# Performance work log

Hardware: AMD Instinct MI355X
Metric: run time of the kernel (lower is better)

The kernel has to match this reference:

```python
import jax, jax.numpy as jnp
import numpy as np

N_NODES = 50000
N_FEAT = 63          # nodeChannels C = N_FEAT + 1 = 64
N_EDGES = 800000
N_LABELS = 10000
BATCH = 4
N_LAYERS = 5
C = N_FEAT + 1


def setup_inputs() -> dict:
    key = jax.random.key(0)
    ks = jax.random.split(key, 16)
    s = 0.05  # small init scale for numerical sanity
    return {
        "cov": jax.random.normal(ks[0], (BATCH, N_LABELS), jnp.float32),
        "nodes": jax.random.normal(ks[1], (N_NODES, N_FEAT), jnp.float32),
        "edges": jax.random.randint(ks[2], (2, N_EDGES), 0, N_NODES, jnp.int64 if jax.config.jax_enable_x64 else jnp.int32),
        "count2label": jnp.arange(N_LABELS, dtype=jnp.int32),
        "ggc_weight": jax.random.normal(ks[3], (N_LAYERS, C, C), jnp.float32) * s,
        "gru_w_ih": jax.random.normal(ks[4], (3 * C, C), jnp.float32) * s,
        "gru_w_hh": jax.random.normal(ks[5], (3 * C, C), jnp.float32) * s,
        "gru_b_ih": jax.random.normal(ks[6], (3 * C,), jnp.float32) * s,
        "gru_b_hh": jax.random.normal(ks[7], (3 * C,), jnp.float32) * s,
        "ai_w": jax.random.normal(ks[8], (2 * C, 2 * C), jnp.float32) * s,
        "ai_b": jax.random.normal(ks[9], (2 * C,), jnp.float32) * s,
        "aj_w": jax.random.normal(ks[10], (2 * C, 2 * C), jnp.float32) * s,
        "aj_b": jax.random.normal(ks[11], (2 * C,), jnp.float32) * s,
        "mlp_w": jax.random.normal(ks[12], (256, 2 * C), jnp.float32) * s,
        "mlp_b": jax.random.normal(ks[13], (256,), jnp.float32) * s,
        "critic_w": jax.random.normal(ks[14], (1, 256), jnp.float32) * s,
        "critic_b": jax.random.normal(ks[15], (1,), jnp.float32) * s,
    }


def _gru_cell(m, h, w_ih, w_hh, b_ih, b_hh):
    # torch GRUCell, gate order r, z, n
    gx = m @ w_ih.T + b_ih   # [..., 3C]
    gh = h @ w_hh.T + b_hh
    c = h.shape[-1]
    xr, xz, xn = gx[..., :c], gx[..., c:2 * c], gx[..., 2 * c:]
    hr, hz, hn = gh[..., :c], gh[..., c:2 * c], gh[..., 2 * c:]
    r = jax.nn.sigmoid(xr + hr)
    z = jax.nn.sigmoid(xz + hz)
    n = jnp.tanh(xn + r * hn)
    return (1.0 - z) * n + z * h


def reference(cov, nodes, edges, count2label, ggc_weight,
              gru_w_ih, gru_w_hh, gru_b_ih, gru_b_hh,
              ai_w, ai_b, aj_w, aj_b, mlp_w, mlp_b, critic_w, critic_b):
    n, f = nodes.shape
    b = cov.shape[0]
    # scatter coverage into per-graph node channel: covInGraph[count2label] = cov
    cov_in_graph = jnp.zeros((b, n), cov.dtype).at[:, count2label].set(cov)
    # batched node input [B, N, C]; batched graph = B identical copies w/ offset edges
    x0 = jnp.concatenate(
        [jnp.broadcast_to(nodes, (b, n, f)), cov_in_graph[..., None]], axis=-1)
    src, dst = edges[0], edges[1]

    def scatter_add(mb):  # [N, C] -> [N, C]: sum messages from source at target
        return jax.ops.segment_sum(mb[src], dst, num_segments=n)

    x = x0
    for i in range(ggc_weight.shape[0]):
        m = x @ ggc_weight[i]                     # dense per-layer matmul [B,N,C]
        agg = jax.vmap(scatter_add)(m)            # edge scatter-add propagate
        x = _gru_cell(agg, x, gru_w_ih, gru_w_hh, gru_b_ih, gru_b_hh)

    # attention gate: sigmoid(Wi cat) * relu(Wj cat), cat = [x, x0]
    cat = jnp.concatenate([x, x0], axis=-1)       # [B, N, 2C]
    att = jax.nn.sigmoid(cat @ ai_w.T + ai_b) * jax.nn.relu(cat @ aj_w.T + aj_b)
    pooled = jax.nn.relu(att.sum(axis=1))         # global_add_pool -> [B, 2C]
    state = jax.nn.relu(pooled @ mlp_w.T + mlp_b) # graphmlp
    return state @ critic_w.T + critic_b          # critic value [B, 1]
```

## Files before the change

kernel.cpp:

```cpp
#include <hip/hip_runtime.h>
#include <math.h>

#define NN 50000
#define NF 63
#define NE 800000
#define NL 10000
#define NB 4
#define NLAY 5
#define BN (NB*NN)
#define NTILES (BN/64)
#define SCAN_NBLK ((NN+255)/256)
#define HIST_NBLK ((NE+255)/256)

using f32x4  = __attribute__((ext_vector_type(4))) float;
using f32x2  = __attribute__((ext_vector_type(2))) float;
using bf16x8 = __attribute__((ext_vector_type(8))) __bf16;

__device__ __forceinline__ float frcp(float x){ return __builtin_amdgcn_rcpf(x); }
__device__ __forceinline__ float sigm(float v){ return frcp(1.f + __expf(-v)); }
__device__ __forceinline__ float tanh_f(float v){ return fmaf(-2.f, frcp(__expf(2.f*v) + 1.f), 1.f); }

__device__ __forceinline__ ushort f2bf(float f){
    uint u = __builtin_bit_cast(uint, f);
    u += 0x7fffu + ((u >> 16) & 1u);
    return (ushort)(u >> 16);
}
__device__ __forceinline__ float bf_lo(uint v){ return __builtin_bit_cast(float, v << 16); }
__device__ __forceinline__ float bfu(ushort v){ return __builtin_bit_cast(float, ((uint)v) << 16); }

__device__ __forceinline__ uchar f2fp8(float v){
    int enc = __builtin_amdgcn_cvt_pk_fp8_f32(v, v, 0, false);
    return (uchar)(enc & 0xff);
}

__device__ __forceinline__ bf16x8 ldfrag(const ushort* p){
    uint4 v = *(const uint4*)p;
    return __builtin_bit_cast(bf16x8, v);
}
__device__ __forceinline__ f32x4 MFMA(bf16x8 a, bf16x8 b, f32x4 c){
    return __builtin_amdgcn_mfma_f32_16x16x32_bf16(a, b, c, 0, 0, 0);
}

__global__ void k_setup(const int* __restrict__ edges, int* __restrict__ cnt,
                        const float* __restrict__ wih, const float* __restrict__ whh,
                        const float* __restrict__ aiw, const float* __restrict__ ajw,
                        const float* __restrict__ ggc,
                        ushort* __restrict__ whhb, ushort* __restrict__ aiwb,
                        ushort* __restrict__ ajwb, ushort* __restrict__ wfb){
    int bid = blockIdx.x;
    if (bid < HIST_NBLK){
        int e = bid*256 + threadIdx.x;
        if (e < NE) atomicAdd(&cnt[edges[NE + e]], 1);
        return;
    }
    int i = (bid - HIST_NBLK)*256 + threadIdx.x;
    if (i < 12288)        whhb[i]        = f2bf(whh[i]);
    else if (i < 28672)   aiwb[i-12288]  = f2bf(aiw[i-12288]);
    else if (i < 45056)   ajwb[i-28672]  = f2bf(ajw[i-28672]);
    else if (i < 106496){
        int t = i - 45056;
        int lay = t / 12288;
        int rem = t % 12288;
        int n = rem >> 6, k = rem & 63;
        const float* W  = ggc + lay*4096 + k*64;
        const float* wr = wih + n*64;
        float s = 0.f;
        #pragma unroll 8
        for (int c = 0; c < 64; ++c) s = fmaf(W[c], wr[c], s);
        wfb[t] = f2bf(s);
    }
}

__global__ void k_scan1(const int* __restrict__ cnt, int* __restrict__ tmp, int* __restrict__ bsum){
    __shared__ int sh[256];
    int tx = threadIdx.x, i = blockIdx.x*256 + tx;
    int v = (i < NN) ? cnt[i] : 0;
    sh[tx] = v; __syncthreads();
    for (int off = 1; off < 256; off <<= 1){
        int u = (tx >= off) ? sh[tx-off] : 0;
        __syncthreads();
        sh[tx] += u;
        __syncthreads();
    }
    int incl = sh[tx];
    if (i < NN) tmp[i] = incl - v;
    if (tx == 255) bsum[blockIdx.x] = incl;
}

__global__ void k_scan2(const int* __restrict__ bsum, int* __restrict__ boff){
    __shared__ int sh[256];
    int tx = threadIdx.x;
    int v = (tx < SCAN_NBLK) ? bsum[tx] : 0;
    sh[tx] = v; __syncthreads();
    for (int off = 1; off < 256; off <<= 1){
        int u = (tx >= off) ? sh[tx-off] : 0;
        __syncthreads();
        sh[tx] += u;
        __syncthreads();
    }
    boff[tx] = sh[tx] - v;
}

__global__ void k_scan3(const int* __restrict__ tmp, const int* __restrict__ boff,
                        int* __restrict__ row_start, int* __restrict__ cursor){
    int i = blockIdx.x*256 + threadIdx.x;
    if (i < NN){
        int rs = tmp[i] + boff[blockIdx.x];
        row_start[i] = rs;
        cursor[i] = rs;
    }
    if (i == 0) row_start[NN] = NE;
}

__global__ void k_fillcsr(const int* __restrict__ edges, int* __restrict__ cursor, int* __restrict__ csr_src){
    int e = blockIdx.x*256 + threadIdx.x;
    if (e < NE){
        int d = edges[NE + e];
        int pos = atomicAdd(&cursor[d], 1);
        csr_src[pos] = edges[e];
    }
}

__global__ void k_x0(const float* __restrict__ nodes, ushort* __restrict__ x0I,
                     uchar* __restrict__ x0F){
    int f = blockIdx.x*256 + threadIdx.x;
    int row = f >> 4, c4 = f & 15;
    int n = row % NN, b = row / NN;
    float v[4];
    #pragma unroll
    for (int i = 0; i < 4; ++i){
        int c = c4*4 + i;
        v[i] = (c < NF) ? nodes[(size_t)n*NF + c] : 0.f;
    }
    uint2 pk;
    pk.x = (uint)f2bf(v[0]) | ((uint)f2bf(v[1]) << 16);
    pk.y = (uint)f2bf(v[2]) | ((uint)f2bf(v[3]) << 16);
    *(uint2*)(x0I + ((size_t)n*4 + b)*64 + c4*4) = pk;
    if (b == 0){
        uint q = 0;
        q = (uint)__builtin_amdgcn_cvt_pk_fp8_f32(v[0], v[1], (int)q, false);
        q = (uint)__builtin_amdgcn_cvt_pk_fp8_f32(v[2], v[3], (int)q, true);
        *(uint*)(x0F + (size_t)n*64 + c4*4) = q;
    }
}

__global__ void k_cov(const float* __restrict__ cov, const int* __restrict__ c2l,
                      ushort* __restrict__ x0I, ushort* __restrict__ covB){
    int i = blockIdx.x*256 + threadIdx.x;
    if (i < NB*NL){
        int b = i / NL, j = i % NL;
        int nd = c2l[j];
        ushort vb = f2bf(cov[i]);
        x0I[((size_t)nd*4 + b)*64 + 63] = vb;
        covB[(size_t)nd*4 + b] = vb;
    }
}

__global__ __launch_bounds__(256) void k_agg0(const uchar* __restrict__ x0F,
                                              const ushort* __restrict__ covB,
                                              const int* __restrict__ row_start,
                                              const int* __restrict__ csr_src,
                                              ushort* __restrict__ aggx){
    int tx = threadIdx.x, l = tx & 63, w = tx >> 6;
    int d = __builtin_amdgcn_readfirstlane(blockIdx.x*4 + w);
    int h = l >> 4;
    int t = l & 15;
    const uint off = (uint)(t*4);
    int e0 = row_start[d], e1 = row_start[d+1];
    float a0=0.f,a1=0.f,a2=0.f,a3=0.f,c=0.f;
    int e = e0 + h;
    for (; e + 12 < e1; e += 16){
        int s[4];
        #pragma unroll
        for (int j = 0; j < 4; ++j) s[j] = csr_src[e + 4*j];
        uint v[4];
        #pragma unroll
        for (int j = 0; j < 4; ++j) v[j] = *(const uint*)(x0F + (size_t)s[j]*64 + off);
        #pragma unroll
        for (int j = 0; j < 4; ++j){
            f32x2 p;
            p = __builtin_amdgcn_cvt_pk_f32_fp8(v[j], false); a0 += p.x; a1 += p.y;
            p = __builtin_amdgcn_cvt_pk_f32_fp8(v[j], true);  a2 += p.x; a3 += p.y;
        }
        if (t < 4){
            #pragma unroll
            for (int j = 0; j < 4; ++j) c += bf_lo((uint)covB[(size_t)s[j]*4 + t]);
        }
    }
    for (; e < e1; e += 4){
        int s0 = csr_src[e];
        uint v0 = *(const uint*)(x0F + (size_t)s0*64 + off);
        f32x2 p;
        p = __builtin_amdgcn_cvt_pk_f32_fp8(v0, false); a0 += p.x; a1 += p.y;
        p = __builtin_amdgcn_cvt_pk_f32_fp8(v0, true);  a2 += p.x; a3 += p.y;
        if (t < 4) c += bf_lo((uint)covB[(size_t)s0*4 + t]);
    }
    a0 += __shfl_xor(a0, 16); a0 += __shfl_xor(a0, 32);
    a1 += __shfl_xor(a1, 16); a1 += __shfl_xor(a1, 32);
    a2 += __shfl_xor(a2, 16); a2 += __shfl_xor(a2, 32);
    a3 += __shfl_xor(a3, 16); a3 += __shfl_xor(a3, 32);
    c  += __shfl_xor(c, 16);  c  += __shfl_xor(c, 32);
    float cb0 = __shfl(c, 0), cb1 = __shfl(c, 1), cb2 = __shfl(c, 2), cb3 = __shfl(c, 3);
    if (h == 0){
        uint2 pk;
        pk.x = (uint)f2bf(a0) | ((uint)f2bf(a1) << 16);
        pk.y = (uint)f2bf(a2) | ((uint)f2bf(a3) << 16);
        float cb[4] = {cb0, cb1, cb2, cb3};
        #pragma unroll
        for (int b = 0; b < 4; ++b){
            uint2 o = pk;
            if (t == 15) o.y = (o.y & 0xffffu) | ((uint)f2bf(cb[b]) << 16);
            *(uint2*)(aggx + (size_t)d*256 + b*64 + t*4) = o;
        }
    }
}

__device__ __forceinline__ void gather4q(const uchar* __restrict__ xF,
                                         const int* __restrict__ row_start,
                                         const int* __restrict__ csr_src,
                                         int d0, int l, ushort* __restrict__ sAgg,
                                         int rbase){
    const int qn = l >> 4;
    const int t  = l & 15;
    const uint off = (uint)(t*16);
    const int d = d0 + qn;
    const int e0 = row_start[d], e1 = row_start[d+1];
    float acc[16];
    #pragma unroll
    for (int k = 0; k < 16; ++k) acc[k] = 0.f;

    int e = e0;
    for (; e + 8 <= e1; e += 8){
        int s[8];
        #pragma unroll
        for (int j = 0; j < 8; ++j) s[j] = csr_src[e + j];
        uint4 v[8];
        #pragma unroll
        for (int j = 0; j < 8; ++j) v[j] = *(const uint4*)(xF + (size_t)s[j]*256 + off);
        #pragma unroll
        for (int j = 0; j < 8; ++j){
            f32x2 p;
            p = __builtin_amdgcn_cvt_pk_f32_fp8(v[j].x, false); acc[0] += p.x; acc[1] += p.y;
            p = __builtin_amdgcn_cvt_pk_f32_fp8(v[j].x, true);  acc[2] += p.x; acc[3] += p.y;
            p = __builtin_amdgcn_cvt_pk_f32_fp8(v[j].y, false); acc[4] += p.x; acc[5] += p.y;
            p = __builtin_amdgcn_cvt_pk_f32_fp8(v[j].y, true);  acc[6] += p.x; acc[7] += p.y;
            p = __builtin_amdgcn_cvt_pk_f32_fp8(v[j].z, false); acc[8] += p.x; acc[9] += p.y;
            p = __builtin_amdgcn_cvt_pk_f32_fp8(v[j].z, true);  acc[10]+= p.x; acc[11]+= p.y;
            p = __builtin_amdgcn_cvt_pk_f32_fp8(v[j].w, false); acc[12]+= p.x; acc[13]+= p.y;
            p = __builtin_amdgcn_cvt_pk_f32_fp8(v[j].w, true);  acc[14]+= p.x; acc[15]+= p.y;
        }
    }
    if (e < e1){
        int s[8];
        #pragma unroll
        for (int j = 0; j < 8; ++j){
            int ee = e + j; if (ee >= e1) ee = e1 - 1;
            s[j] = csr_src[ee];
        }
        uint4 v[8];
        #pragma unroll
        for (int j = 0; j < 8; ++j){
            v[j] = *(const uint4*)(xF + (size_t)s[j]*256 + off);
            if (e + j >= e1) v[j] = (uint4){0u,0u,0u,0u};
        }
        #pragma unroll
        for (int j = 0; j < 8; ++j){
            f32x2 p;
            p = __builtin_amdgcn_cvt_pk_f32_fp8(v[j].x, false); acc[0] += p.x; acc[1] += p.y;
            p = __builtin_amdgcn_cvt_pk_f32_fp8(v[j].x, true);  acc[2] += p.x; acc[3] += p.y;
            p = __builtin_amdgcn_cvt_pk_f32_fp8(v[j].y, false); acc[4] += p.x; acc[5] += p.y;
            p = __builtin_amdgcn_cvt_pk_f32_fp8(v[j].y, true);  acc[6] += p.x; acc[7] += p.y;
            p = __builtin_amdgcn_cvt_pk_f32_fp8(v[j].z, false); acc[8] += p.x; acc[9] += p.y;
            p = __builtin_amdgcn_cvt_pk_f32_fp8(v[j].z, true);  acc[10]+= p.x; acc[11]+= p.y;
            p = __builtin_amdgcn_cvt_pk_f32_fp8(v[j].w, false); acc[12]+= p.x; acc[13]+= p.y;
            p = __builtin_amdgcn_cvt_pk_f32_fp8(v[j].w, true);  acc[14]+= p.x; acc[15]+= p.y;
        }
    }

    const int row = rbase + qn*4 + (t >> 2);
    const int c0  = (t & 3)*16;
    uint4 o0, o1;
    o0.x = (uint)f2bf(acc[0])  | ((uint)f2bf(acc[1])  << 16);
    o0.y = (uint)f2bf(acc[2])  | ((uint)f2bf(acc[3])  << 16);
    o0.z = (uint)f2bf(acc[4])  | ((uint)f2bf(acc[5])  << 16);
    o0.w = (uint)f2bf(acc[6])  | ((uint)f2bf(acc[7])  << 16);
    o1.x = (uint)f2bf(acc[8])  | ((uint)f2bf(acc[9])  << 16);
    o1.y = (uint)f2bf(acc[10]) | ((uint)f2bf(acc[11]) << 16);
    o1.z = (uint)f2bf(acc[12]) | ((uint)f2bf(acc[13]) << 16);
    o1.w = (uint)f2bf(acc[14]) | ((uint)f2bf(acc[15]) << 16);
    *(uint4*)(&sAgg[(size_t)row*72 + c0])     = o0;
    *(uint4*)(&sAgg[(size_t)row*72 + c0 + 8]) = o1;
}

__device__ __forceinline__ void gru_core(const ushort* sAgg, const ushort* sX,
                                         const ushort* __restrict__ wfb, const ushort* __restrict__ whhb,
                                         const float* __restrict__ bih, const float* __restrict__ bhh,
                                         int li, int q, int n0, float xv[4][4]){
    f32x4 Cr[4], Cz[4], Cxn[4], Chn[4];
    #pragma unroll
    for (int m = 0; m < 4; ++m){
        Cr[m]=(f32x4){0.f,0.f,0.f,0.f}; Cz[m]=(f32x4){0.f,0.f,0.f,0.f};
        Cxn[m]=(f32x4){0.f,0.f,0.f,0.f}; Chn[m]=(f32x4){0.f,0.f,0.f,0.f};
    }
    #pragma unroll
    for (int ks = 0; ks < 4; ++ks){
        const ushort* wb = (ks < 2) ? wfb : whhb;
        const ushort* sT = (ks < 2) ? sAgg : sX;
        const int kb = (ks & 1)*32;
        bf16x8 Br = ldfrag(wb + (size_t)(n0 + li)*64 + kb + q*8);
        bf16x8 Bz = ldfrag(wb + (size_t)(64 + n0 + li)*64 + kb + q*8);
        bf16x8 Bn = ldfrag(wb + (size_t)(128 + n0 + li)*64 + kb + q*8);
        #pragma unroll
        for (int m = 0; m < 4; ++m){
            bf16x8 A = ldfrag(&sT[(m*16 + li)*72 + kb + q*8]);
            Cr[m] = MFMA(A, Br, Cr[m]);
            Cz[m] = MFMA(A, Bz, Cz[m]);
            if (ks < 2) Cxn[m] = MFMA(A, Bn, Cxn[m]);
            else        Chn[m] = MFMA(A, Bn, Chn[m]);
        }
    }
    const int c = n0 + li;
    const float br_ = bih[c]     + bhh[c];
    const float bz_ = bih[64+c]  + bhh[64+c];
    const float bn_ = bih[128+c];
    const float bh_ = bhh[128+c];
    #pragma unroll
    for (int m = 0; m < 4; ++m){
        #pragma unroll
        for (int rg = 0; rg < 4; ++rg){
            int rl = m*16 + q*4 + rg;
            float r = sigm(Cr[m][rg] + br_);
            float z = sigm(Cz[m][rg] + bz_);
            float nng = tanh_f(Cxn[m][rg] + bn_ + r*(Chn[m][rg] + bh_));
            xv[m][rg] = (1.f - z)*nng + z*bfu(sX[rl*72 + c]);
        }
    }
}

__global__ __launch_bounds__(256) void k_gruF(const ushort* __restrict__ xsrc,
                                              const ushort* __restrict__ aggx,
                                              const ushort* __restrict__ wfb, const ushort* __restrict__ whhb,
                                              const float* __restrict__ bih, const float* __restrict__ bhh,
                                              ushort* __restrict__ xout, uchar* __restrict__ xFout){
    __shared__ __align__(16) ushort sAgg[64*72];
    __shared__ __align__(16) ushort sX[64*72];
    const int tx = threadIdx.x;
    const int l  = tx & 63, li = l & 15, q = l >> 4;
    const int w  = __builtin_amdgcn_readfirstlane(tx >> 6);
    const int R0 = blockIdx.x*64;

    #pragma unroll
    for (int it = 0; it < 2; ++it){
        int idx = it*256 + tx, r = idx >> 3, g = idx & 7;
        size_t go = (size_t)(R0 + r)*64 + g*8;
        *(uint4*)(&sAgg[r*72 + g*8]) = *(const uint4*)(aggx + go);
        *(uint4*)(&sX[r*72 + g*8])   = *(const uint4*)(xsrc + go);
    }
    __syncthreads();

    float xv[4][4];
    gru_core(sAgg, sX, wfb, whhb, bih, bhh, li, q, 16*w, xv);

    const int c = 16*w + li;
    #pragma unroll
    for (int m = 0; m < 4; ++m)
        #pragma unroll
        for (int rg = 0; rg < 4; ++rg){
            size_t ro = (size_t)(R0 + m*16 + q*4 + rg)*64 + c;
            xout[ro]  = f2bf(xv[m][rg]);
            xFout[ro] = f2fp8(xv[m][rg]);
        }
}

__global__ __launch_bounds__(256) void k_gruFf(const uchar* __restrict__ xFin,
                                               const int* __restrict__ row_start,
                                               const int* __restrict__ csr_src,
                                               const ushort* __restrict__ xsrc,
                                               const ushort* __restrict__ wfb, const ushort* __restrict__ whhb,
                                               const float* __restrict__ bih, const float* __restrict__ bhh,
                                               ushort* __restrict__ xout, uchar* __restrict__ xFout){
    __shared__ __align__(16) ushort sAgg[64*72];
    __shared__ __align__(16) ushort sX[64*72];
    const int tx = threadIdx.x;
    const int l  = tx & 63, li = l & 15, q = l >> 4;
    const int w  = __builtin_amdgcn_readfirstlane(tx >> 6);
    const int R0 = blockIdx.x*64;

    #pragma unroll
    for (int it = 0; it < 2; ++it){
        int idx = it*256 + tx, r = idx >> 3, g = idx & 7;
        *(uint4*)(&sX[r*72 + g*8]) = *(const uint4*)(xsrc + (size_t)(R0 + r)*64 + g*8);
    }
    gather4q(xFin, row_start, csr_src, blockIdx.x*16 + w*4, l, sAgg, w*16);
    __syncthreads();

    float xv[4][4];
    gru_core(sAgg, sX, wfb, whhb, bih, bhh, li, q, 16*w, xv);

    const int c = 16*w + li;
    #pragma unroll
    for (int m = 0; m < 4; ++m)
        #pragma unroll
        for (int rg = 0; rg < 4; ++rg){
            size_t ro = (size_t)(R0 + m*16 + q*4 + rg)*64 + c;
            xout[ro]  = f2bf(xv[m][rg]);
            xFout[ro] = f2fp8(xv[m][rg]);
        }
}

__global__ __launch_bounds__(256) void k_gruLf(const uchar* __restrict__ xFin,
                                               const int* __restrict__ row_start,
                                               const int* __restrict__ csr_src,
                                               const ushort* __restrict__ xsrc,
                                               const ushort* __restrict__ wfb, const ushort* __restrict__ whhb,
                                               const float* __restrict__ bih, const float* __restrict__ bhh,
                                               const ushort* __restrict__ x0I,
                                               const ushort* __restrict__ aiwb, const float* __restrict__ aib,
                                               const ushort* __restrict__ ajwb, const float* __restrict__ ajb,
                                               float* __restrict__ pooled16){
    __shared__ __align__(16) ushort sAgg[64*72];
    __shared__ __align__(16) ushort sX[64*72];
    const int tx = threadIdx.x;
    const int l  = tx & 63, li = l & 15, q = l >> 4;
    const int w  = __builtin_amdgcn_readfirstlane(tx >> 6);
    const int R0 = blockIdx.x*64;

    #pragma unroll
    for (int it = 0; it < 2; ++it){
        int idx = it*256 + tx, r = idx >> 3, g = idx & 7;
        *(uint4*)(&sX[r*72 + g*8]) = *(const uint4*)(xsrc + (size_t)(R0 + r)*64 + g*8);
    }
    gather4q(xFin, row_start, csr_src, blockIdx.x*16 + w*4, l, sAgg, w*16);
    __syncthreads();

    float xv[4][4];
    gru_core(sAgg, sX, wfb, whhb, bih, bhh, li, q, 16*w, xv);
    __syncthreads();

    const int c = 16*w + li;
    #pragma unroll
    for (int m = 0; m < 4; ++m)
        #pragma unroll
        for (int rg = 0; rg < 4; ++rg)
            sAgg[(m*16 + q*4 + rg)*72 + c] = f2bf(xv[m][rg]);
    #pragma unroll
    for (int it = 0; it < 2; ++it){
        int idx = it*256 + tx, r = idx >> 3, g = idx & 7;
        *(uint4*)(&sX[r*72 + g*8]) = *(const uint4*)(x0I + (size_t)(R0 + r)*64 + g*8);
    }
    __syncthreads();

    f32x4 Ai[2][4], Aj[2][4];
    #pragma unroll
    for (int t = 0; t < 2; ++t)
        #pragma unroll
        for (int m = 0; m < 4; ++m){ Ai[t][m]=(f32x4){0.f,0.f,0.f,0.f}; Aj[t][m]=(f32x4){0.f,0.f,0.f,0.f}; }

    const int nb0 = 32*w;
    #pragma unroll
    for (int ks = 0; ks < 4; ++ks){
        const ushort* sT = (ks < 2) ? sAgg : sX;
        const int kb = (ks & 1)*32;
        bf16x8 Bi[2], Bj[2];
        #pragma unroll
        for (int t = 0; t < 2; ++t){
            Bi[t] = ldfrag(aiwb + (size_t)(nb0 + 16*t + li)*128 + ks*32 + q*8);
            Bj[t] = ldfrag(ajwb + (size_t)(nb0 + 16*t + li)*128 + ks*32 + q*8);
        }
        #pragma unroll
        for (int m = 0; m < 4; ++m){
            bf16x8 A = ldfrag(&sT[(m*16 + li)*72 + kb + q*8]);
            #pragma unroll
            for (int t = 0; t < 2; ++t){
                Ai[t][m] = MFMA(A, Bi[t], Ai[t][m]);
                Aj[t][m] = MFMA(A, Bj[t], Aj[t][m]);
            }
        }
    }

    float* pb = pooled16 + (size_t)(blockIdx.x & 15)*512;
    #pragma unroll
    for (int t = 0; t < 2; ++t){
        int cc = nb0 + 16*t + li;
        float bia = aib[cc], bja = ajb[cc];
        float vs[4] = {0.f, 0.f, 0.f, 0.f};
        #pragma unroll
        for (int m = 0; m < 4; ++m){
            #pragma unroll
            for (int rg = 0; rg < 4; ++rg){
                float s = sigm(Ai[t][m][rg] + bia);
                float a = Aj[t][m][rg] + bja;
                a = a > 0.f ? a : 0.f;
                vs[rg] += s*a;
            }
        }
        #pragma unroll
        for (int b = 0; b < 4; ++b){
            vs[b] += __shfl_xor(vs[b], 16);
            vs[b] += __shfl_xor(vs[b], 32);
        }
        if (l < 16){
            #pragma unroll
            for (int b = 0; b < 4; ++b) atomicAdd(&pb[b*128 + nb0 + 16*t + l], vs[b]);
        }
    }
}

__global__ void k_final(const float* __restrict__ pooled16, const float* __restrict__ mw,
                        const float* __restrict__ mb, const float* __restrict__ cw,
                        const float* __restrict__ cb, float* __restrict__ out){
    __shared__ float red[256];
    int t = threadIdx.x;
    int b = blockIdx.x;
    float acc = mb[t];
    #pragma unroll 4
    for (int k = 0; k < 128; ++k){
        float p = 0.f;
        #pragma unroll
        for (int kb = 0; kb < 16; ++kb) p += pooled16[kb*512 + b*128 + k];
        p = p > 0.f ? p : 0.f;
        acc = fmaf(p, mw[t*128 + k], acc);
    }
    float st = acc > 0.f ? acc : 0.f;
    red[t] = st * cw[t];
    __syncthreads();
    for (int off = 128; off > 0; off >>= 1){
        if (t < off) red[t] += red[t + off];
        __syncthreads();
    }
    if (t == 0) out[b] = red[0] + cb[0];
}

extern "C" void kernel_launch(void* const* d_in, const int* in_sizes, int n_in,
                              void* d_out, int out_size, void* d_ws, size_t ws_size,
                              hipStream_t stream) {
    const float* cov   = (const float*)d_in[0];
    const float* nodes = (const float*)d_in[1];
    const int*   edges = (const int*)d_in[2];
    const int*   c2l   = (const int*)d_in[3];
    const float* ggc   = (const float*)d_in[4];
    const float* wih   = (const float*)d_in[5];
    const float* whh   = (const float*)d_in[6];
    const float* bih   = (const float*)d_in[7];
    const float* bhh   = (const float*)d_in[8];
    const float* aiw   = (const float*)d_in[9];
    const float* aib   = (const float*)d_in[10];
    const float* ajw   = (const float*)d_in[11];
    const float* ajb   = (const float*)d_in[12];
    const float* mlpw  = (const float*)d_in[13];
    const float* mlpb  = (const float*)d_in[14];
    const float* cw    = (const float*)d_in[15];
    const float* cb    = (const float*)d_in[16];
    float* out = (float*)d_out;

    const size_t XSZ = (size_t)BN * 64;
    float* ws = (float*)d_ws;
    float* pooled16 = ws;
    ushort* xS    = (ushort*)(pooled16 + 8192);
    ushort* x0I   = xS + XSZ;
    ushort* aggx  = x0I + XSZ;
    ushort* covB  = aggx + XSZ;
    ushort* whhb  = covB + (size_t)NN*4;
    ushort* aiwb  = whhb + 12288;
    ushort* ajwb  = aiwb + 16384;
    ushort* wfb   = ajwb + 16384;
    uchar* xF     = (uchar*)(wfb + 61440);
    uchar* x0F    = xF + XSZ;
    int* cnt       = (int*)(x0F + (size_t)NN*64);
    int* tmp       = cnt + NN;
    int* bsum      = tmp + NN;
    int* boff      = bsum + 256;
    int* row_start = boff + 256;
    int* cursor    = row_start + (NN + 1);
    int* csr_src   = cursor + NN;

    hipMemsetAsync(cnt, 0, (size_t)NN*sizeof(int), stream);
    hipMemsetAsync(pooled16, 0, 8192*sizeof(float), stream);
    hipMemsetAsync(covB, 0, (size_t)NN*4*sizeof(ushort), stream);

    k_setup<<<HIST_NBLK + 416, 256, 0, stream>>>(edges, cnt, wih, whh, aiw, ajw, ggc,
                                                 whhb, aiwb, ajwb, wfb);
    k_scan1<<<SCAN_NBLK, 256, 0, stream>>>(cnt, tmp, bsum);
    k_scan2<<<1, 256, 0, stream>>>(bsum, boff);
    k_scan3<<<SCAN_NBLK, 256, 0, stream>>>(tmp, boff, row_start, cursor);
    k_fillcsr<<<(NE + 255)/256, 256, 0, stream>>>(edges, cursor, csr_src);

    k_x0<<<(BN*16)/256, 256, 0, stream>>>(nodes, x0I, x0F);
    k_cov<<<(NB*NL + 255)/256, 256, 0, stream>>>(cov, c2l, x0I, covB);

    uchar* xFbuf[2] = { xF, (uchar*)aggx };

    for (int i = 0; i < NLAY; ++i){
        const ushort* wf = wfb + (size_t)i*12288;
        if (i == 0){
            k_agg0<<<NN/4, 256, 0, stream>>>(x0F, covB, row_start, csr_src, aggx);
            k_gruF<<<NTILES, 256, 0, stream>>>(x0I, aggx, wf, whhb, bih, bhh, xS, xFbuf[0]);
        } else if (i < NLAY - 1){
            k_gruFf<<<NTILES, 256, 0, stream>>>(xFbuf[(i+1)&1], row_start, csr_src, xS,
                                                wf, whhb, bih, bhh, xS, xFbuf[i&1]);
        } else {
            k_gruLf<<<NTILES, 256, 0, stream>>>(xFbuf[(i+1)&1], row_start, csr_src, xS,
                                                wf, whhb, bih, bhh,
                                                x0I, aiwb, aib, ajwb, ajb, pooled16);
        }
    }

    k_final<<<NB, 256, 0, stream>>>(pooled16, mlpw, mlpb, cw, cb, out);
    (void)in_sizes; (void)n_in; (void)out_size; (void)ws_size;
}
```

Baseline: 586.5 us.

## Fuse layer-0 aggregation into GRU kernel and stage CSR indices in LDS

Replaces the separate layer-0 aggregation kernel plus GRU kernel with a single fused kernel that gathers fp8 x0 rows and coverage directly into shared memory, removing one launch and the aggx global round trip. All gather kernels now preload the block's CSR source indices into a 1024-entry LDS buffer, falling back to global reads when the block has more edges than that. It also uses packed f32x2 accumulation and raises wave priority around the MFMA loops. The extra LDS and barrier may reduce occupancy.

```diff
diff --git a/kernel.cpp b/kernel.cpp
--- a/kernel.cpp
+++ b/kernel.cpp
@@ -156,68 +156,70 @@
     }
 }
 
-__global__ __launch_bounds__(256) void k_agg0(const uchar* __restrict__ x0F,
-                                              const ushort* __restrict__ covB,
-                                              const int* __restrict__ row_start,
-                                              const int* __restrict__ csr_src,
-                                              ushort* __restrict__ aggx){
-    int tx = threadIdx.x, l = tx & 63, w = tx >> 6;
-    int d = __builtin_amdgcn_readfirstlane(blockIdx.x*4 + w);
-    int h = l >> 4;
-    int t = l & 15;
+template<bool LI>
+__device__ __forceinline__ void gather0q(const uchar* __restrict__ x0F,
+                                         const ushort* __restrict__ covB,
+                                         const int* __restrict__ row_start,
+                                         const int* __restrict__ csr_src,
+                                         const int* sIdx, int estart,
+                                         int d0, int l, ushort* __restrict__ sAgg,
+                                         int rbase){
+    const int qn = l >> 4, t = l & 15;
     const uint off = (uint)(t*4);
-    int e0 = row_start[d], e1 = row_start[d+1];
-    float a0=0.f,a1=0.f,a2=0.f,a3=0.f,c=0.f;
-    int e = e0 + h;
-    for (; e + 12 < e1; e += 16){
-        int s[4];
-        #pragma unroll
-        for (int j = 0; j < 4; ++j) s[j] = csr_src[e + 4*j];
-        uint v[4];
-        #pragma unroll
-        for (int j = 0; j < 4; ++j) v[j] = *(const uint*)(x0F + (size_t)s[j]*64 + off);
-        #pragma unroll
-        for (int j = 0; j < 4; ++j){
-            f32x2 p;
-            p = __builtin_amdgcn_cvt_pk_f32_fp8(v[j], false); a0 += p.x; a1 += p.y;
-            p = __builtin_amdgcn_cvt_pk_f32_fp8(v[j], true);  a2 += p.x; a3 += p.y;
+    const int d = d0 + qn;
+    const int e0 = row_start[d], e1 = row_start[d+1];
+    f32x2 a01 = (f32x2){0.f,0.f}, a23 = (f32x2){0.f,0.f};
+    float c = 0.f;
+    int e = e0;
+    for (; e + 8 <= e1; e += 8){
+        int s[8];
+        #pragma unroll
+        for (int j = 0; j < 8; ++j) s[j] = LI ? sIdx[e + j - estart] : csr_src[e + j];
+        uint v[8];
+        #pragma unroll
+        for (int j = 0; j < 8; ++j) v[j] = *(const uint*)(x0F + (size_t)s[j]*64 + off);
+        #pragma unroll
+        for (int j = 0; j < 8; ++j){
+            a01 += __builtin_amdgcn_cvt_pk_f32_fp8(v[j], false);
+            a23 += __builtin_amdgcn_cvt_pk_f32_fp8(v[j], true);
         }
         if (t < 4){
             #pragma unroll
-            for (int j = 0; j < 4; ++j) c += bf_lo((uint)covB[(size_t)s[j]*4 + t]);
-        }
-    }
-    for (; e < e1; e += 4){
-        int s0 = csr_src[e];
-        uint v0 = *(const uint*)(x0F + (size_t)s0*64 + off);
-        f32x2 p;
-        p = __builtin_amdgcn_cvt_pk_f32_fp8(v0, false); a0 += p.x; a1 += p.y;
-        p = __builtin_amdgcn_cvt_pk_f32_fp8(v0, true);  a2 += p.x; a3 += p.y;
-        if (t < 4) c += bf_lo((uint)covB[(size_t)s0*4 + t]);
-    }
-    a0 += __shfl_xor(a0, 16); a0 += __shfl_xor(a0, 32);
-    a1 += __shfl_xor(a1, 16); a1 += __shfl_xor(a1, 32);
-    a2 += __shfl_xor(a2, 16); a2 += __shfl_xor(a2, 32);
-    a3 += __shfl_xor(a3, 16); a3 += __shfl_xor(a3, 32);
-    c  += __shfl_xor(c, 16);  c  += __shfl_xor(c, 32);
-    float cb0 = __shfl(c, 0), cb1 = __shfl(c, 1), cb2 = __shfl(c, 2), cb3 = __shfl(c, 3);
-    if (h == 0){
-        uint2 pk;
-        pk.x = (uint)f2bf(a0) | ((uint)f2bf(a1) << 16);
-        pk.y = (uint)f2bf(a2) | ((uint)f2bf(a3) << 16);
-        float cb[4] = {cb0, cb1, cb2, cb3};
-        #pragma unroll
-        for (int b = 0; b < 4; ++b){
-            uint2 o = pk;
-            if (t == 15) o.y = (o.y & 0xffffu) | ((uint)f2bf(cb[b]) << 16);
-            *(uint2*)(aggx + (size_t)d*256 + b*64 + t*4) = o;
-        }
-    }
-}
-
+            for (int j = 0; j < 8; ++j) c += bf_lo((uint)covB[(size_t)s[j]*4 + t]);
+        }
+    }
+    if (e < e1){
+        #pragma unroll
+        for (int j = 0; j < 8; ++j){
+            int ee = e + j; bool ok = ee < e1; if (!ok) ee = e1 - 1;
+            int s = LI ? sIdx[ee - estart] : csr_src[ee];
+            uint v = *(const uint*)(x0F + (size_t)s*64 + off);
+            if (!ok) v = 0u;
+            a01 += __builtin_amdgcn_cvt_pk_f32_fp8(v, false);
+            a23 += __builtin_amdgcn_cvt_pk_f32_fp8(v, true);
+            if (t < 4){
+                float cv = bf_lo((uint)covB[(size_t)s*4 + t]);
+                c += ok ? cv : 0.f;
+            }
+        }
+    }
+    uint2 pk;
+    pk.x = (uint)f2bf(a01.x) | ((uint)f2bf(a01.y) << 16);
+    pk.y = (uint)f2bf(a23.x) | ((uint)f2bf(a23.y) << 16);
+    #pragma unroll
+    for (int b = 0; b < 4; ++b){
+        float cb = __shfl(c, (l & 48) | b);
+        uint2 o = pk;
+        if (t == 15) o.y = (o.y & 0xffffu) | ((uint)f2bf(cb) << 16);
+        *(uint2*)(&sAgg[(size_t)(rbase + qn*4 + b)*72 + t*4]) = o;
+    }
+}
+
+template<bool LI>
 __device__ __forceinline__ void gather4q(const uchar* __restrict__ xF,
                                          const int* __restrict__ row_start,
                                          const int* __restrict__ csr_src,
+                                         const int* sIdx, int estart,
                                          int d0, int l, ushort* __restrict__ sAgg,
                                          int rbase){
     const int qn = l >> 4;
@@ -225,69 +227,59 @@
     const uint off = (uint)(t*16);
     const int d = d0 + qn;
     const int e0 = row_start[d], e1 = row_start[d+1];
-    float acc[16];
-    #pragma unroll
-    for (int k = 0; k < 16; ++k) acc[k] = 0.f;
+    f32x2 ac[8];
+    #pragma unroll
+    for (int k = 0; k < 8; ++k) ac[k] = (f32x2){0.f,0.f};
 
     int e = e0;
     for (; e + 8 <= e1; e += 8){
         int s[8];
         #pragma unroll
-        for (int j = 0; j < 8; ++j) s[j] = csr_src[e + j];
+        for (int j = 0; j < 8; ++j) s[j] = LI ? sIdx[e + j - estart] : csr_src[e + j];
         uint4 v[8];
         #pragma unroll
         for (int j = 0; j < 8; ++j) v[j] = *(const uint4*)(xF + (size_t)s[j]*256 + off);
         #pragma unroll
         for (int j = 0; j < 8; ++j){
-            f32x2 p;
-            p = __builtin_amdgcn_cvt_pk_f32_fp8(v[j].x, false); acc[0] += p.x; acc[1] += p.y;
-            p = __builtin_amdgcn_cvt_pk_f32_fp8(v[j].x, true);  acc[2] += p.x; acc[3] += p.y;
-            p = __builtin_amdgcn_cvt_pk_f32_fp8(v[j].y, false); acc[4] += p.x; acc[5] += p.y;
-            p = __builtin_amdgcn_cvt_pk_f32_fp8(v[j].y, true);  acc[6] += p.x; acc[7] += p.y;
-            p = __builtin_amdgcn_cvt_pk_f32_fp8(v[j].z, false); acc[8] += p.x; acc[9] += p.y;
-            p = __builtin_amdgcn_cvt_pk_f32_fp8(v[j].z, true);  acc[10]+= p.x; acc[11]+= p.y;
-            p = __builtin_amdgcn_cvt_pk_f32_fp8(v[j].w, false); acc[12]+= p.x; acc[13]+= p.y;
-            p = __builtin_amdgcn_cvt_pk_f32_fp8(v[j].w, true);  acc[14]+= p.x; acc[15]+= p.y;
+            ac[0] += __builtin_amdgcn_cvt_pk_f32_fp8(v[j].x, false);
+            ac[1] += __builtin_amdgcn_cvt_pk_f32_fp8(v[j].x, true);
+            ac[2] += __builtin_amdgcn_cvt_pk_f32_fp8(v[j].y, false);
+            ac[3] += __builtin_amdgcn_cvt_pk_f32_fp8(v[j].y, true);
+            ac[4] += __builtin_amdgcn_cvt_pk_f32_fp8(v[j].z, false);
+            ac[5] += __builtin_amdgcn_cvt_pk_f32_fp8(v[j].z, true);
+            ac[6] += __builtin_amdgcn_cvt_pk_f32_fp8(v[j].w, false);
+            ac[7] += __builtin_amdgcn_cvt_pk_f32_fp8(v[j].w, true);
         }
     }
     if (e < e1){
-        int s[8];
         #pragma unroll
         for (int j = 0; j < 8; ++j){
-            int ee = e + j; if (ee >= e1) ee = e1 - 1;
-            s[j] = csr_src[ee];
-        }
-        uint4 v[8];
-        #pragma unroll
-        for (int j = 0; j < 8; ++j){
-            v[j] = *(const uint4*)(xF + (size_t)s[j]*256 + off);
-            if (e + j >= e1) v[j] = (uint4){0u,0u,0u,0u};
-        }
-        #pragma unroll
-        for (int j = 0; j < 8; ++j){
-            f32x2 p;
-            p = __builtin_amdgcn_cvt_pk_f32_fp8(v[j].x, false); acc[0] += p.x; acc[1] += p.y;
-            p = __builtin_amdgcn_cvt_pk_f32_fp8(v[j].x, true);  acc[2] += p.x; acc[3] += p.y;
-            p = __builtin_amdgcn_cvt_pk_f32_fp8(v[j].y, false); acc[4] += p.x; acc[5] += p.y;
-            p = __builtin_amdgcn_cvt_pk_f32_fp8(v[j].y, true);  acc[6] += p.x; acc[7] += p.y;
-            p = __builtin_amdgcn_cvt_pk_f32_fp8(v[j].z, false); acc[8] += p.x; acc[9] += p.y;
-            p = __builtin_amdgcn_cvt_pk_f32_fp8(v[j].z, true);  acc[10]+= p.x; acc[11]+= p.y;
-            p = __builtin_amdgcn_cvt_pk_f32_fp8(v[j].w, false); acc[12]+= p.x; acc[13]+= p.y;
-            p = __builtin_amdgcn_cvt_pk_f32_fp8(v[j].w, true);  acc[14]+= p.x; acc[15]+= p.y;
+            int ee = e + j; bool ok = ee < e1; if (!ok) ee = e1 - 1;
+            int s = LI ? sIdx[ee - estart] : csr_src[ee];
+            uint4 v = *(const uint4*)(xF + (size_t)s*256 + off);
+            if (!ok) v = (uint4){0u,0u,0u,0u};
+            ac[0] += __builtin_amdgcn_cvt_pk_f32_fp8(v.x, false);
+            ac[1] += __builtin_amdgcn_cvt_pk_f32_fp8(v.x, true);
+            ac[2] += __builtin_amdgcn_cvt_pk_f32_fp8(v.y, false);
+            ac[3] += __builtin_amdgcn_cvt_pk_f32_fp8(v.y, true);
+            ac[4] += __builtin_amdgcn_cvt_pk_f32_fp8(v.z, false);
+            ac[5] += __builtin_amdgcn_cvt_pk_f32_fp8(v.z, true);
+            ac[6] += __builtin_amdgcn_cvt_pk_f32_fp8(v.w, false);
+            ac[7] += __builtin_amdgcn_cvt_pk_f32_fp8(v.w, true);
         }
     }
 
     const int row = rbase + qn*4 + (t >> 2);
     const int c0  = (t & 3)*16;
     uint4 o0, o1;
-    o0.x = (uint)f2bf(acc[0])  | ((uint)f2bf(acc[1])  << 16);
-    o0.y = (uint)f2bf(acc[2])  | ((uint)f2bf(acc[3])  << 16);
-    o0.z = (uint)f2bf(acc[4])  | ((uint)f2bf(acc[5])  << 16);
-    o0.w = (uint)f2bf(acc[6])  | ((uint)f2bf(acc[7])  << 16);
-    o1.x = (uint)f2bf(acc[8])  | ((uint)f2bf(acc[9])  << 16);
-    o1.y = (uint)f2bf(acc[10]) | ((uint)f2bf(acc[11]) << 16);
-    o1.z = (uint)f2bf(acc[12]) | ((uint)f2bf(acc[13]) << 16);
-    o1.w = (uint)f2bf(acc[14]) | ((uint)f2bf(acc[15]) << 16);
+    o0.x = (uint)f2bf(ac[0].x) | ((uint)f2bf(ac[0].y) << 16);
+    o0.y = (uint)f2bf(ac[1].x) | ((uint)f2bf(ac[1].y) << 16);
+    o0.z = (uint)f2bf(ac[2].x) | ((uint)f2bf(ac[2].y) << 16);
+    o0.w = (uint)f2bf(ac[3].x) | ((uint)f2bf(ac[3].y) << 16);
+    o1.x = (uint)f2bf(ac[4].x) | ((uint)f2bf(ac[4].y) << 16);
+    o1.y = (uint)f2bf(ac[5].x) | ((uint)f2bf(ac[5].y) << 16);
+    o1.z = (uint)f2bf(ac[6].x) | ((uint)f2bf(ac[6].y) << 16);
+    o1.w = (uint)f2bf(ac[7].x) | ((uint)f2bf(ac[7].y) << 16);
     *(uint4*)(&sAgg[(size_t)row*72 + c0])     = o0;
     *(uint4*)(&sAgg[(size_t)row*72 + c0 + 8]) = o1;
 }
@@ -302,6 +294,7 @@
         Cr[m]=(f32x4){0.f,0.f,0.f,0.f}; Cz[m]=(f32x4){0.f,0.f,0.f,0.f};
         Cxn[m]=(f32x4){0.f,0.f,0.f,0.f}; Chn[m]=(f32x4){0.f,0.f,0.f,0.f};
     }
+    __builtin_amdgcn_s_setprio(1);
     #pragma unroll
     for (int ks = 0; ks < 4; ++ks){
         const ushort* wb = (ks < 2) ? wfb : whhb;
@@ -319,6 +312,7 @@
             else        Chn[m] = MFMA(A, Bn, Chn[m]);
         }
     }
+    __builtin_amdgcn_s_setprio(0);
     const int c = n0 + li;
     const float br_ = bih[c]     + bhh[c];
     const float bz_ = bih[64+c]  + bhh[64+c];
@@ -337,25 +331,35 @@
     }
 }
 
-__global__ __launch_bounds__(256) void k_gruF(const ushort* __restrict__ xsrc,
-                                              const ushort* __restrict__ aggx,
-                                              const ushort* __restrict__ wfb, const ushort* __restrict__ whhb,
-                                              const float* __restrict__ bih, const float* __restrict__ bhh,
-                                              ushort* __restrict__ xout, uchar* __restrict__ xFout){
+__global__ __launch_bounds__(256) void k_gru0f(const uchar* __restrict__ x0F,
+                                               const ushort* __restrict__ covB,
+                                               const int* __restrict__ row_start,
+                                               const int* __restrict__ csr_src,
+                                               const ushort* __restrict__ x0I,
+                                               const ushort* __restrict__ wfb, const ushort* __restrict__ whhb,
+                                               const float* __restrict__ bih, const float* __restrict__ bhh,
+                                               ushort* __restrict__ xout, uchar* __restrict__ xFout){
     __shared__ __align__(16) ushort sAgg[64*72];
     __shared__ __align__(16) ushort sX[64*72];
+    __shared__ int sIdx[1024];
     const int tx = threadIdx.x;
     const int l  = tx & 63, li = l & 15, q = l >> 4;
     const int w  = __builtin_amdgcn_readfirstlane(tx >> 6);
     const int R0 = blockIdx.x*64;
+    const int n0 = blockIdx.x*16;
+    const int estart = row_start[n0], eend = row_start[n0 + 16];
+    const int ecnt = eend - estart;
 
     #pragma unroll
     for (int it = 0; it < 2; ++it){
         int idx = it*256 + tx, r = idx >> 3, g = idx & 7;
-        size_t go = (size_t)(R0 + r)*64 + g*8;
-        *(uint4*)(&sAgg[r*72 + g*8]) = *(const uint4*)(aggx + go);
-        *(uint4*)(&sX[r*72 + g*8])   = *(const uint4*)(xsrc + go);
-    }
+        *(uint4*)(&sX[r*72 + g*8]) = *(const uint4*)(x0I + (size_t)(R0 + r)*64 + g*8);
+    }
+    for (int k = tx; k < ecnt && k < 1024; k += 256) sIdx[k] = csr_src[estart + k];
+    __syncthreads();
+
+    if (ecnt <= 1024) gather0q<true >(x0F, covB, row_start, csr_src, sIdx, estart, n0 + w*4, l, sAgg, w*16);
+    else              gather0q<false>(x0F, covB, row_start, csr_src, sIdx, estart, n0 + w*4, l, sAgg, w*16);
     __syncthreads();
 
     float xv[4][4];
@@ -381,17 +385,25 @@
                                                ushort* __restrict__ xout, uchar* __restrict__ xFout){
     __shared__ __align__(16) ushort sAgg[64*72];
     __shared__ __align__(16) ushort sX[64*72];
+    __shared__ int sIdx[1024];
     const int tx = threadIdx.x;
     const int l  = tx & 63, li = l & 15, q = l >> 4;
     const int w  = __builtin_amdgcn_readfirstlane(tx >> 6);
     const int R0 = blockIdx.x*64;
+    const int n0 = blockIdx.x*16;
+    const int estart = row_start[n0], eend = row_start[n0 + 16];
+    const int ecnt = eend - estart;
 
     #pragma unroll
     for (int it = 0; it < 2; ++it){
         int idx = it*256 + tx, r = idx >> 3, g = idx & 7;
         *(uint4*)(&sX[r*72 + g*8]) = *(const uint4*)(xsrc + (size_t)(R0 + r)*64 + g*8);
     }
-    gather4q(xFin, row_start, csr_src, blockIdx.x*16 + w*4, l, sAgg, w*16);
+    for (int k = tx; k < ecnt && k < 1024; k += 256) sIdx[k] = csr_src[estart + k];
+    __syncthreads();
+
+    if (ecnt <= 1024) gather4q<true >(xFin, row_start, csr_src, sIdx, estart, n0 + w*4, l, sAgg, w*16);
+    else              gather4q<false>(xFin, row_start, csr_src, sIdx, estart, n0 + w*4, l, sAgg, w*16);
     __syncthreads();
 
     float xv[4][4];
@@ -420,17 +432,25 @@
                                                float* __restrict__ pooled16){
     __shared__ __align__(16) ushort sAgg[64*72];
     __shared__ __align__(16) ushort sX[64*72];
+    __shared__ int sIdx[1024];
     const int tx = threadIdx.x;
     const int l  = tx & 63, li = l & 15, q = l >> 4;
     const int w  = __builtin_amdgcn_readfirstlane(tx >> 6);
     const int R0 = blockIdx.x*64;
+    const int n0 = blockIdx.x*16;
+    const int estart = row_start[n0], eend = row_start[n0 + 16];
+    const int ecnt = eend - estart;
 
     #pragma unroll
     for (int it = 0; it < 2; ++it){
         int idx = it*256 + tx, r = idx >> 3, g = idx & 7;
         *(uint4*)(&sX[r*72 + g*8]) = *(const uint4*)(xsrc + (size_t)(R0 + r)*64 + g*8);
     }
-    gather4q(xFin, row_start, csr_src, blockIdx.x*16 + w*4, l, sAgg, w*16);
+    for (int k = tx; k < ecnt && k < 1024; k += 256) sIdx[k] = csr_src[estart + k];
+    __syncthreads();
+
+    if (ecnt <= 1024) gather4q<true >(xFin, row_start, csr_src, sIdx, estart, n0 + w*4, l, sAgg, w*16);
+    else              gather4q<false>(xFin, row_start, csr_src, sIdx, estart, n0 + w*4, l, sAgg, w*16);
     __syncthreads();
 
     float xv[4][4];
@@ -457,6 +477,7 @@
         for (int m = 0; m < 4; ++m){ Ai[t][m]=(f32x4){0.f,0.f,0.f,0.f}; Aj[t][m]=(f32x4){0.f,0.f,0.f,0.f}; }
 
     const int nb0 = 32*w;
+    __builtin_amdgcn_s_setprio(1);
     #pragma unroll
     for (int ks = 0; ks < 4; ++ks){
         const ushort* sT = (ks < 2) ? sAgg : sX;
@@ -477,6 +498,7 @@
             }
         }
     }
+    __builtin_amdgcn_s_setprio(0);
 
     float* pb = pooled16 + (size_t)(blockIdx.x & 15)*512;
     #pragma unroll
@@ -593,8 +615,8 @@
     for (int i = 0; i < NLAY; ++i){
         const ushort* wf = wfb + (size_t)i*12288;
         if (i == 0){
-            k_agg0<<<NN/4, 256, 0, stream>>>(x0F, covB, row_start, csr_src, aggx);
-            k_gruF<<<NTILES, 256, 0, stream>>>(x0I, aggx, wf, whhb, bih, bhh, xS, xFbuf[0]);
+            k_gru0f<<<NTILES, 256, 0, stream>>>(x0F, covB, row_start, csr_src, x0I,
+                                                wf, whhb, bih, bhh, xS, xFbuf[0]);
         } else if (i < NLAY - 1){
             k_gruFf<<<NTILES, 256, 0, stream>>>(xFbuf[(i+1)&1], row_start, csr_src, xS,
                                                 wf, whhb, bih, bhh, xS, xFbuf[i&1]);
```

Measured after the change: 568.8 us. 1.03x faster.
